# Kernel optimization log

Measured on AMD Instinct MI355X. Metric: run time of the kernel, lower is better.

The kernel has to match this reference:

```python
import jax, jax.numpy as jnp
import numpy as np

B, N, K, E, H, V = 128, 256, 4, 300, 150, 32000  # batch, nodes/tree, max children, embed, hidden, vocab
DELTA = 1.0


def setup_inputs() -> dict:
    key = jax.random.key(0)
    ks = jax.random.split(key, 8)
    query = jax.random.randint(ks[0], (B, N), 0, V, dtype=jnp.int32)
    pos = jax.random.randint(ks[1], (B, N), 0, V, dtype=jnp.int32)
    neg = jax.random.randint(ks[2], (B, N), 0, V, dtype=jnp.int32)
    # Complete K-ary tree over N nodes: children of node t are {K*t+1, ..., K*t+K} < N; root = node 0.
    ch = np.full((N, K), -1, dtype=np.int32)
    for t in range(N):
        for j in range(K):
            c = K * t + 1 + j
            if c < N:
                ch[t, j] = c
    children = jnp.asarray(ch)
    emb = jax.random.normal(ks[3], (V, E), dtype=jnp.float32) * 0.02
    W_iou = jax.random.normal(ks[4], (E, 3 * H), dtype=jnp.float32) * 0.05
    U_iou = jax.random.normal(ks[5], (H, 3 * H), dtype=jnp.float32) * 0.05
    b_iou = jnp.zeros((3 * H,), jnp.float32)
    W_f = jax.random.normal(ks[6], (E, H), dtype=jnp.float32) * 0.05
    U_f = jax.random.normal(ks[7], (H, H), dtype=jnp.float32) * 0.05
    b_f = jnp.zeros((H,), jnp.float32)
    return {"query": query, "pos": pos, "neg": neg, "children": children,
            "emb": emb, "W_iou": W_iou, "U_iou": U_iou, "b_iou": b_iou,
            "W_f": W_f, "U_f": U_f, "b_f": b_f}


def _childsum_treelstm(x, children, W_iou, U_iou, b_iou, W_f, U_f, b_f):
    """x: [B, N, E] node embeddings. Returns root (c, h): each [B, H]."""
    Bn, Nn, _ = x.shape
    Hh = U_f.shape[0]
    h0 = jnp.zeros((Bn, Nn, Hh), x.dtype)
    c0 = jnp.zeros((Bn, Nn, Hh), x.dtype)

    def step(carry, t):
        h_all, c_all = carry
        ch = children[t]                        # [K] child indices, -1 = padding
        mask = (ch >= 0)
        idx = jnp.where(mask, ch, 0)
        m = mask.astype(x.dtype)[None, :, None]  # [1, K, 1]
        h_k = h_all[:, idx] * m                 # [B, K, H]
        c_k = c_all[:, idx] * m
        h_sum = h_k.sum(axis=1)                 # child-sum h_tilde [B, H]
        x_t = x[:, t]                           # [B, E]
        iou = x_t @ W_iou + h_sum @ U_iou + b_iou
        i, o, u = jnp.split(iou, 3, axis=-1)
        i = jax.nn.sigmoid(i)
        o = jax.nn.sigmoid(o)
        u = jnp.tanh(u)
        # per-child forget gates: f_jk = sigmoid(W_f x_j + U_f h_k + b_f)
        f = jax.nn.sigmoid((x_t @ W_f + b_f)[:, None, :] + h_k @ U_f)  # [B, K, H]
        c_t = i * u + (f * c_k).sum(axis=1)     # c_k already masked
        h_t = o * jnp.tanh(c_t)
        return (h_all.at[:, t].set(h_t), c_all.at[:, t].set(c_t)), None

    # children have larger indices than parents -> process N-1 .. 0 (root last)
    (h_all, c_all), _ = jax.lax.scan(step, (h0, c0), jnp.arange(Nn - 1, -1, -1))
    return c_all[:, 0], h_all[:, 0]


def _cosine(a, b):
    num = (a * b).sum(-1)
    den = jnp.sqrt((a * a).sum(-1) * (b * b).sum(-1)) + 1e-8
    return num / den


def reference(query, pos, neg, children, emb, W_iou, U_iou, b_iou, W_f, U_f, b_f):
    qc, _ = _childsum_treelstm(emb[query], children, W_iou, U_iou, b_iou, W_f, U_f, b_f)
    pc, _ = _childsum_treelstm(emb[pos], children, W_iou, U_iou, b_iou, W_f, U_f, b_f)
    nc, _ = _childsum_treelstm(emb[neg], children, W_iou, U_iou, b_iou, W_f, U_f, b_f)
    a = _cosine(qc, pc)  # [B]
    b = _cosine(qc, nc)  # [B]
    return jax.nn.relu(DELTA - a + b)
```

## Files before the change

### kernel.cpp

```cpp
#include <hip/hip_runtime.h>
#include <hip/hip_bf16.h>

typedef short short8 __attribute__((ext_vector_type(8)));
typedef float floatx4 __attribute__((ext_vector_type(4)));
typedef unsigned short ushort;

#define Bb 128
#define Nn 256
#define Hh 150
#define HK 160
#define Vv 32000
#define NROW 384
#define PROJC 600
#define NINT 64
#define ZROW (Vv + NROW * NINT)

#define WTN 640

__device__ __forceinline__ float sigf(float x) { return 1.0f / (1.0f + __expf(-x)); }
__device__ __forceinline__ float tanhf_(float x) { return 1.0f - 2.0f / (__expf(2.0f * x) + 1.0f); }
__device__ __forceinline__ float bf2f(ushort s) { union { float f; unsigned u; } v; v.u = ((unsigned)s) << 16; return v.f; }
__device__ __forceinline__ ushort f2bf(float f) { __hip_bfloat16 h = __float2bfloat16(f); return *(ushort*)&h; }

__global__ __launch_bounds__(256) void k_prep(
    const float* __restrict__ W_iou, const float* __restrict__ W_f,
    const float* __restrict__ U_iou, const float* __restrict__ U_f,
    const float* __restrict__ b_iou, const float* __restrict__ b_f,
    short* __restrict__ Wt, short* __restrict__ Uti, short* __restrict__ Utf,
    float* __restrict__ biasw, ushort* __restrict__ h_u, float* __restrict__ c_u)
{
    int idx = blockIdx.x * 256 + threadIdx.x;
    const int nWt = WTN * 320, nUi = 464 * 160, nUf = 160 * 160;
    if (idx < nWt) {
        int n = idx / 320, k = idx % 320;
        float v = 0.f;
        if (k < 300) { if (n < 450) v = W_iou[k * 450 + n]; else if (n < 600) v = W_f[k * 150 + (n - 450)]; }
        Wt[idx] = (short)f2bf(v);
    } else if (idx < nWt + nUi) {
        int i2 = idx - nWt; int n = i2 / 160, k = i2 % 160;
        float v = (k < 150 && n < 450) ? U_iou[k * 450 + n] : 0.f;
        Uti[i2] = (short)f2bf(v);
    } else if (idx < nWt + nUi + nUf) {
        int i2 = idx - nWt - nUi; int n = i2 / 160, k = i2 % 160;
        float v = (k < 150) ? U_f[k * 150 + n] : 0.f;
        Utf[i2] = (short)f2bf(v);
    } else if (idx < nWt + nUi + nUf + WTN) {
        int n = idx - nWt - nUi - nUf;
        biasw[n] = n < 450 ? b_iou[n] : (n < 600 ? b_f[n - 450] : 0.f);
    } else if (idx < nWt + nUi + nUf + WTN + HK) {
        int k = idx - (nWt + nUi + nUf + WTN);
        h_u[(long)ZROW * HK + k] = 0;
        c_u[(long)ZROW * HK + k] = 0.f;
    }
}

__global__ __launch_bounds__(256) void k_vproj(
    const float* __restrict__ emb, const short* __restrict__ Wt,
    const float* __restrict__ biasw, ushort* __restrict__ proj)
{
    __shared__ __align__(16) short As[2][32][328];
    const int tid = threadIdx.x;
    const int cg = blockIdx.x % 10;
    const int rg = blockIdx.x / 10;
    const int rowbase = rg * 320;

    const int w = tid >> 6, lane = tid & 63;
    const int m = lane & 15, kq = (lane >> 4) * 8;
    const int tile = cg * 4 + w;
    const int col = tile * 16 + m;

    short8 bq[10];
    #pragma unroll
    for (int ks = 0; ks < 10; ks++)
        bq[ks] = *(const short8*)(Wt + (long)col * 320 + kq + ks * 32);
    const float bias = biasw[col];

    for (int i = tid; i < 2 * 32 * 5; i += 256) {
        int bz = i / 160, r2 = (i % 160) / 5, kk = (i % 5) * 4;
        *(short4*)&As[bz][r2][300 + kk] = make_short4(0, 0, 0, 0);
    }

    {
        const float4* src = (const float4*)emb + (long)rowbase * 75;
        for (int i = tid; i < 2400; i += 256) {
            int r = i / 75, k0 = (i % 75) * 4;
            float4 x = src[i];
            short4 sv;
            sv.x = (short)f2bf(x.x); sv.y = (short)f2bf(x.y);
            sv.z = (short)f2bf(x.z); sv.w = (short)f2bf(x.w);
            *(short4*)&As[0][r][k0] = sv;
        }
    }
    __syncthreads();

    for (int c = 0; c < 10; c++) {
        const int buf = c & 1;

        float4 x[10];
        if (c < 9) {
            const float4* src = (const float4*)emb + (long)(rowbase + (c + 1) * 32) * 75;
            #pragma unroll
            for (int j = 0; j < 10; j++) {
                int i = tid + j * 256;
                if (i < 2400) x[j] = src[i];
            }
        }

        floatx4 acc0 = {0.f, 0.f, 0.f, 0.f}, acc1 = {0.f, 0.f, 0.f, 0.f};
        #pragma unroll
        for (int ks = 0; ks < 10; ks++) {
            short8 a0 = *(const short8*)&As[buf][m][kq + ks * 32];
            short8 a1 = *(const short8*)&As[buf][16 + m][kq + ks * 32];
            acc0 = __builtin_amdgcn_mfma_f32_16x16x32_bf16(a0, bq[ks], acc0, 0, 0, 0);
            acc1 = __builtin_amdgcn_mfma_f32_16x16x32_bf16(a1, bq[ks], acc1, 0, 0, 0);
        }

        if (col < PROJC) {
            int v0 = rowbase + c * 32;
            int rb = (lane >> 4) * 4;
            #pragma unroll
            for (int reg = 0; reg < 4; reg++) {
                proj[(long)(v0 + rb + reg) * PROJC + col]      = f2bf(acc0[reg] + bias);
                proj[(long)(v0 + 16 + rb + reg) * PROJC + col] = f2bf(acc1[reg] + bias);
            }
        }

        if (c < 9) {
            #pragma unroll
            for (int j = 0; j < 10; j++) {
                int i = tid + j * 256;
                if (i < 2400) {
                    int r = i / 75, k0 = (i % 75) * 4;
                    short4 sv;
                    sv.x = (short)f2bf(x[j].x); sv.y = (short)f2bf(x[j].y);
                    sv.z = (short)f2bf(x[j].z); sv.w = (short)f2bf(x[j].w);
                    *(short4*)&As[buf ^ 1][r][k0] = sv;
                }
            }
        }
        __syncthreads();
    }
}

__global__ __launch_bounds__(256) void k_vleaf(
    const ushort* __restrict__ proj, ushort* __restrict__ h_u, float* __restrict__ c_u)
{
    int idx = blockIdx.x * 256 + threadIdx.x;
    int v = idx / 20, k0 = (idx % 20) * 8;
    const ushort* pr = proj + (long)v * PROJC;
    ushort hv[8]; float cvv[8];
    #pragma unroll
    for (int e = 0; e < 8; e++) {
        int k = k0 + e;
        if (k < Hh) {
            float iv = sigf(bf2f(pr[k]));
            float ov = sigf(bf2f(pr[150 + k]));
            float uv = tanhf_(bf2f(pr[300 + k]));
            float cc = iv * uv;
            cvv[e] = cc;
            hv[e] = f2bf(ov * tanhf_(cc));
        } else { cvv[e] = 0.f; hv[e] = 0; }
    }
    *(int4*)(h_u + (long)v * HK + k0) = *(int4*)hv;
    *(float4*)(c_u + (long)v * HK + k0)     = make_float4(cvv[0], cvv[1], cvv[2], cvv[3]);
    *(float4*)(c_u + (long)v * HK + k0 + 4) = make_float4(cvv[4], cvv[5], cvv[6], cvv[7]);
}

__global__ __launch_bounds__(256) void k_level(
    int t0,
    const int* __restrict__ tq, const int* __restrict__ tp, const int* __restrict__ tn,
    const int* __restrict__ children, const ushort* __restrict__ proj,
    const short* __restrict__ Uti, const short* __restrict__ Utf,
    ushort* __restrict__ h_u, float* __restrict__ c_u)
{
    __shared__ __align__(16) short As[5][16][168];
    __shared__ int idx_s[16][4];
    __shared__ int tok_s[16];

    const int tid = threadIdx.x;
    const int t = t0 + blockIdx.x / 24;
    const int r0 = (blockIdx.x % 24) * 16;

    if (tid < 64) {
        int r = tid >> 2, j = tid & 3;
        int rg = r0 + r, g = rg >> 7, b = rg & 127;
        const int* tok = (g == 0) ? tq : (g == 1 ? tp : tn);
        int ch = children[t * 4 + j];
        int idx;
        if (ch < 0)        idx = ZROW;
        else if (ch >= 64) idx = tok[b * Nn + ch];
        else               idx = Vv + rg * NINT + ch;
        idx_s[r][j] = idx;
        if (j == 0) tok_s[r] = tok[b * Nn + t];
    }
    __syncthreads();

    for (int i = tid; i < 16 * 20; i += 256) {
        int r = i / 20, k0 = (i % 20) * 8;
        int4 v0 = *(const int4*)(h_u + (long)idx_s[r][0] * HK + k0);
        int4 v1 = *(const int4*)(h_u + (long)idx_s[r][1] * HK + k0);
        int4 v2 = *(const int4*)(h_u + (long)idx_s[r][2] * HK + k0);
        int4 v3 = *(const int4*)(h_u + (long)idx_s[r][3] * HK + k0);
        *(int4*)&As[1][r][k0] = v0;
        *(int4*)&As[2][r][k0] = v1;
        *(int4*)&As[3][r][k0] = v2;
        *(int4*)&As[4][r][k0] = v3;
        ushort s[8];
        const ushort* p0 = (const ushort*)&v0; const ushort* p1 = (const ushort*)&v1;
        const ushort* p2 = (const ushort*)&v2; const ushort* p3 = (const ushort*)&v3;
        #pragma unroll
        for (int e = 0; e < 8; e++)
            s[e] = f2bf(bf2f(p0[e]) + bf2f(p1[e]) + bf2f(p2[e]) + bf2f(p3[e]));
        *(int4*)&As[0][r][k0] = *(int4*)s;
    }
    __syncthreads();

    const int w = tid >> 6, lane = tid & 63;
    const int m = lane & 15, kq = (lane >> 4) * 8;

    for (int nt = w; nt < 10; nt += 4) {
        int col = nt * 16 + m;
        const short* bi  = Uti + (long)(col) * HK + kq;
        const short* bo  = Uti + (long)(150 + col) * HK + kq;
        const short* bu  = Uti + (long)(300 + col) * HK + kq;
        const short* bff = Utf + (long)col * HK + kq;
        floatx4 ai = {0.f,0.f,0.f,0.f}, ao = ai, au = ai;
        floatx4 af0 = ai, af1 = ai, af2 = ai, af3 = ai;
        #pragma unroll
        for (int ks = 0; ks < 5; ks++) {
            short8 asum = *(const short8*)&As[0][m][kq + ks * 32];
            short8 ac0  = *(const short8*)&As[1][m][kq + ks * 32];
            short8 ac1  = *(const short8*)&As[2][m][kq + ks * 32];
            short8 ac2  = *(const short8*)&As[3][m][kq + ks * 32];
            short8 ac3  = *(const short8*)&As[4][m][kq + ks * 32];
            short8 vbi = *(const short8*)(bi + ks * 32);
            short8 vbo = *(const short8*)(bo + ks * 32);
            short8 vbu = *(const short8*)(bu + ks * 32);
            short8 vbf = *(const short8*)(bff + ks * 32);
            ai  = __builtin_amdgcn_mfma_f32_16x16x32_bf16(asum, vbi, ai, 0, 0, 0);
            ao  = __builtin_amdgcn_mfma_f32_16x16x32_bf16(asum, vbo, ao, 0, 0, 0);
            au  = __builtin_amdgcn_mfma_f32_16x16x32_bf16(asum, vbu, au, 0, 0, 0);
            af0 = __builtin_amdgcn_mfma_f32_16x16x32_bf16(ac0,  vbf, af0, 0, 0, 0);
            af1 = __builtin_amdgcn_mfma_f32_16x16x32_bf16(ac1,  vbf, af1, 0, 0, 0);
            af2 = __builtin_amdgcn_mfma_f32_16x16x32_bf16(ac2,  vbf, af2, 0, 0, 0);
            af3 = __builtin_amdgcn_mfma_f32_16x16x32_bf16(ac3,  vbf, af3, 0, 0, 0);
        }

        int rbase = (lane >> 4) * 4;
        if (col < Hh) {
            #pragma unroll
            for (int reg = 0; reg < 4; reg++) {
                int r = rbase + reg, rg = r0 + r;
                const ushort* pr = proj + (long)tok_s[r] * PROJC;
                float iv = sigf(bf2f(pr[col])        + ai[reg]);
                float ov = sigf(bf2f(pr[150 + col])  + ao[reg]);
                float uv = tanhf_(bf2f(pr[300 + col]) + au[reg]);
                float fpre = bf2f(pr[450 + col]);
                float cv = iv * uv;
                cv = fmaf(sigf(fpre + af0[reg]), c_u[(long)idx_s[r][0] * HK + col], cv);
                cv = fmaf(sigf(fpre + af1[reg]), c_u[(long)idx_s[r][1] * HK + col], cv);
                cv = fmaf(sigf(fpre + af2[reg]), c_u[(long)idx_s[r][2] * HK + col], cv);
                cv = fmaf(sigf(fpre + af3[reg]), c_u[(long)idx_s[r][3] * HK + col], cv);
                long o = (long)(Vv + rg * NINT + t) * HK + col;
                c_u[o] = cv;
                h_u[o] = f2bf(ov * tanhf_(cv));
            }
        } else {
            #pragma unroll
            for (int reg = 0; reg < 4; reg++) {
                long o = (long)(Vv + (r0 + rbase + reg) * NINT + t) * HK + col;
                c_u[o] = 0.f; h_u[o] = 0;
            }
        }
    }
}

__global__ __launch_bounds__(64) void k_cos(const float* __restrict__ c_u, float* __restrict__ out)
{
    int b = blockIdx.x, tid = threadIdx.x;
    const float* qc = c_u + (long)(Vv + (0 * Bb + b) * NINT) * HK;
    const float* pc = c_u + (long)(Vv + (1 * Bb + b) * NINT) * HK;
    const float* nc = c_u + (long)(Vv + (2 * Bb + b) * NINT) * HK;
    float qp = 0, qn = 0, qq = 0, pp = 0, nn2 = 0;
    for (int k = tid; k < Hh; k += 64) {
        float qv = qc[k], pv = pc[k], nv = nc[k];
        qp += qv * pv; qn += qv * nv; qq += qv * qv; pp += pv * pv; nn2 += nv * nv;
    }
    #pragma unroll
    for (int off = 32; off > 0; off >>= 1) {
        qp += __shfl_down(qp, off, 64);
        qn += __shfl_down(qn, off, 64);
        qq += __shfl_down(qq, off, 64);
        pp += __shfl_down(pp, off, 64);
        nn2 += __shfl_down(nn2, off, 64);
    }
    if (tid == 0) {
        float a = qp / (sqrtf(qq * pp) + 1e-8f);
        float d = qn / (sqrtf(qq * nn2) + 1e-8f);
        out[b] = fmaxf(0.0f, 1.0f - a + d);
    }
}

extern "C" void kernel_launch(void* const* d_in, const int* in_sizes, int n_in,
                              void* d_out, int out_size, void* d_ws, size_t ws_size,
                              hipStream_t stream)
{
    const int*   tq       = (const int*)d_in[0];
    const int*   tp       = (const int*)d_in[1];
    const int*   tn       = (const int*)d_in[2];
    const int*   children = (const int*)d_in[3];
    const float* emb      = (const float*)d_in[4];
    const float* W_iou    = (const float*)d_in[5];
    const float* U_iou    = (const float*)d_in[6];
    const float* b_iou    = (const float*)d_in[7];
    const float* W_f      = (const float*)d_in[8];
    const float* U_f      = (const float*)d_in[9];
    const float* b_f      = (const float*)d_in[10];
    float* out = (float*)d_out;

    char* ws = (char*)d_ws;
    ushort* proj  = (ushort*)ws;
    ushort* h_u   = (ushort*)(ws + 38400000);
    float*  c_u   = (float*)(ws + 56504640);
    short*  Wt    = (short*)(ws + 92713920);
    short*  Uti   = (short*)(ws + 93123520);
    short*  Utf   = (short*)(ws + 93272000);
    float*  biasw = (float*)(ws + 93323200);

    k_prep<<<1194, 256, 0, stream>>>(W_iou, W_f, U_iou, U_f, b_iou, b_f,
                                     Wt, Uti, Utf, biasw, h_u, c_u);
    k_vproj<<<1000, 256, 0, stream>>>(emb, Wt, biasw, proj);
    k_vleaf<<<2500, 256, 0, stream>>>(proj, h_u, c_u);
    k_level<<<43 * 24, 256, 0, stream>>>(21, tq, tp, tn, children, proj, Uti, Utf, h_u, c_u);
    k_level<<<16 * 24, 256, 0, stream>>>(5,  tq, tp, tn, children, proj, Uti, Utf, h_u, c_u);
    k_level<<<4 * 24, 256, 0, stream>>>(1,   tq, tp, tn, children, proj, Uti, Utf, h_u, c_u);
    k_level<<<1 * 24, 256, 0, stream>>>(0,   tq, tp, tn, children, proj, Uti, Utf, h_u, c_u);
    k_cos<<<Bb, 64, 0, stream>>>(c_u, out);
}
```

Before: 270.8 us.

## Double column tiles per wave in vocab projection and remap blocks across XCDs

Each wave in the vocabulary projection kernel now computes two 16-column tiles instead of one. This halves the block count and halves how often each block loads and converts the embedding rows to bf16, since every staged A tile now feeds twice as many MFMAs. Block IDs are also remapped so consecutive work groups, which share the same embedding rows, land on the same XCD for better L2 locality. The cost is twice the B-operand registers per thread, which may lower occupancy, and fewer blocks to spread across the GPU.

```diff
diff --git a/kernel.cpp b/kernel.cpp
--- a/kernel.cpp
+++ b/kernel.cpp
@@ -60,20 +60,29 @@
 {
     __shared__ __align__(16) short As[2][32][328];
     const int tid = threadIdx.x;
-    const int cg = blockIdx.x % 10;
-    const int rg = blockIdx.x / 10;
+
+    const int bid = blockIdx.x;
+    const int xcd = bid & 7, li = bid >> 3;
+    const int wgid = (xcd < 4 ? xcd * 63 : 252 + (xcd - 4) * 62) + li;
+
+    const int cg = wgid % 5;
+    const int rg = wgid / 5;
     const int rowbase = rg * 320;
 
     const int w = tid >> 6, lane = tid & 63;
     const int m = lane & 15, kq = (lane >> 4) * 8;
-    const int tile = cg * 4 + w;
-    const int col = tile * 16 + m;
-
-    short8 bq[10];
+    const int t0 = cg * 8 + w * 2;
+    const int col0 = t0 * 16 + m;
+    const int col1 = col0 + 16;
+
+    short8 bq0[10], bq1[10];
     #pragma unroll
-    for (int ks = 0; ks < 10; ks++)
-        bq[ks] = *(const short8*)(Wt + (long)col * 320 + kq + ks * 32);
-    const float bias = biasw[col];
+    for (int ks = 0; ks < 10; ks++) {
+        bq0[ks] = *(const short8*)(Wt + (long)col0 * 320 + kq + ks * 32);
+        bq1[ks] = *(const short8*)(Wt + (long)col1 * 320 + kq + ks * 32);
+    }
+    const float bias0 = biasw[col0];
+    const float bias1 = biasw[col1];
 
     for (int i = tid; i < 2 * 32 * 5; i += 256) {
         int bz = i / 160, r2 = (i % 160) / 5, kk = (i % 5) * 4;
@@ -106,22 +115,33 @@
             }
         }
 
-        floatx4 acc0 = {0.f, 0.f, 0.f, 0.f}, acc1 = {0.f, 0.f, 0.f, 0.f};
+        floatx4 a00 = {0.f,0.f,0.f,0.f}, a01 = a00, a10 = a00, a11 = a00;
         #pragma unroll
         for (int ks = 0; ks < 10; ks++) {
             short8 a0 = *(const short8*)&As[buf][m][kq + ks * 32];
             short8 a1 = *(const short8*)&As[buf][16 + m][kq + ks * 32];
-            acc0 = __builtin_amdgcn_mfma_f32_16x16x32_bf16(a0, bq[ks], acc0, 0, 0, 0);
-            acc1 = __builtin_amdgcn_mfma_f32_16x16x32_bf16(a1, bq[ks], acc1, 0, 0, 0);
-        }
-
-        if (col < PROJC) {
+            a00 = __builtin_amdgcn_mfma_f32_16x16x32_bf16(a0, bq0[ks], a00, 0, 0, 0);
+            a01 = __builtin_amdgcn_mfma_f32_16x16x32_bf16(a0, bq1[ks], a01, 0, 0, 0);
+            a10 = __builtin_amdgcn_mfma_f32_16x16x32_bf16(a1, bq0[ks], a10, 0, 0, 0);
+            a11 = __builtin_amdgcn_mfma_f32_16x16x32_bf16(a1, bq1[ks], a11, 0, 0, 0);
+        }
+
+        {
             int v0 = rowbase + c * 32;
             int rb = (lane >> 4) * 4;
-            #pragma unroll
-            for (int reg = 0; reg < 4; reg++) {
-                proj[(long)(v0 + rb + reg) * PROJC + col]      = f2bf(acc0[reg] + bias);
-                proj[(long)(v0 + 16 + rb + reg) * PROJC + col] = f2bf(acc1[reg] + bias);
+            if (col0 < PROJC) {
+                #pragma unroll
+                for (int reg = 0; reg < 4; reg++) {
+                    proj[(long)(v0 + rb + reg) * PROJC + col0]      = f2bf(a00[reg] + bias0);
+                    proj[(long)(v0 + 16 + rb + reg) * PROJC + col0] = f2bf(a10[reg] + bias0);
+                }
+            }
+            if (col1 < PROJC) {
+                #pragma unroll
+                for (int reg = 0; reg < 4; reg++) {
+                    proj[(long)(v0 + rb + reg) * PROJC + col1]      = f2bf(a01[reg] + bias1);
+                    proj[(long)(v0 + 16 + rb + reg) * PROJC + col1] = f2bf(a11[reg] + bias1);
+                }
             }
         }
 
@@ -329,7 +349,7 @@
 
     k_prep<<<1194, 256, 0, stream>>>(W_iou, W_f, U_iou, U_f, b_iou, b_f,
                                      Wt, Uti, Utf, biasw, h_u, c_u);
-    k_vproj<<<1000, 256, 0, stream>>>(emb, Wt, biasw, proj);
+    k_vproj<<<500, 256, 0, stream>>>(emb, Wt, biasw, proj);
     k_vleaf<<<2500, 256, 0, stream>>>(proj, h_u, c_u);
     k_level<<<43 * 24, 256, 0, stream>>>(21, tq, tp, tn, children, proj, Uti, Utf, h_u, c_u);
     k_level<<<16 * 24, 256, 0, stream>>>(5,  tq, tp, tn, children, proj, Uti, Utf, h_u, c_u);
```

Measured after the change: 252.2 us. 6.9% less time.
